# Optimization experiments

Hardware: AMD Instinct MI355X
Metric: run time of the kernel (lower is better)

Reference implementation:

```python
import jax, jax.numpy as jnp
import numpy as np
from jax import lax

STRIDES = (8, 16, 32)
NUM_CLASSES = 80
TOPK = 1000
CONF_THRESH = 0.05
NMS_THRESH = 0.6


def setup_inputs() -> dict:
    key = jax.random.key(0)
    ks = jax.random.split(key, 10)
    hw = [(256, 256), (128, 128), (64, 64)]
    inp = {}
    for lv, (h, w) in enumerate(hw):
        inp[f"cls_pred_{lv}"] = jax.random.normal(ks[3 * lv + 0], (NUM_CLASSES, h, w), jnp.float32)
        inp[f"reg_pred_{lv}"] = jax.random.normal(ks[3 * lv + 1], (4, h, w), jnp.float32)
        inp[f"ctn_pred_{lv}"] = jax.random.normal(ks[3 * lv + 2], (1, h, w), jnp.float32)
    inp["scales"] = jax.random.uniform(ks[9], (3,), jnp.float32)
    return inp


def _level_decode(cls_p, reg_p, ctn_p, scale, stride):
    # cls_p: [C,H,W] -> flatten to [M,C] matching torch permute(1,2,0).view(-1,C)
    C, H, W = cls_p.shape
    cls = jnp.transpose(cls_p, (1, 2, 0)).reshape(-1, C)          # [M,C]
    reg = jnp.transpose(reg_p, (1, 2, 0)).reshape(-1, 4)          # [M,4]
    reg = jax.nn.relu(reg * scale) * stride                       # Scale + relu + stride
    ctn = jnp.transpose(ctn_p, (1, 2, 0)).reshape(-1, 1)          # [M,1]
    joint = jnp.sqrt(jax.nn.sigmooid(cls) * jax.nn.sigmoid(ctn)) if False else \
        jnp.sqrt(jax.nn.sigmoid(cls) * jax.nn.sigmoid(ctn))      # [M,C]
    scores = jnp.max(joint, axis=-1)                              # [M]
    labels = jnp.argmax(joint, axis=-1)                           # [M]
    ay, ax = jnp.meshgrid(jnp.arange(H), jnp.arange(W), indexing='ij')
    anchors = (jnp.stack([ax, ay], -1).reshape(-1, 2).astype(cls.dtype) + 0.5) * stride  # [M,2]
    # per-level topk (M > TOPK for all levels here)
    scores, idx = lax.top_k(scores, TOPK)
    labels = labels[idx]
    reg = reg[idx]
    anchors = anchors[idx]
    boxes = jnp.concatenate([anchors - reg[:, :2], anchors + reg[:, 2:]], axis=-1)  # x1y1x2y2
    return scores, labels, boxes


def _nms(boxes, scores):
    # Faithful port of the pure-python NMS: fixed-shape keep mask, sorted order.
    N = boxes.shape[0]
    order = jnp.argsort(-scores)
    b = boxes[order]
    x1, y1, x2, y2 = b[:, 0], b[:, 1], b[:, 2], b[:, 3]
    areas = (x2 - x1) * (y2 - y1)
    xx1 = jnp.maximum(x1[:, None], x1[None, :])
    yy1 = jnp.maximum(y1[:, None], y1[None, :])
    xx2 = jnp.minimum(x2[:, None], x2[None, :])
    yy2 = jnp.minimum(y2[:, None], y2[None, :])
    w = jnp.maximum(1e-10, xx2 - xx1)
    h = jnp.maximum(1e-10, yy2 - yy1)
    inter = w * h
    iou = inter / (areas[:, None] + areas[None, :] - inter + 1e-14)  # [N,N]
    idxs = jnp.arange(N)

    def body(i, keep):
        sup = (iou[i] > NMS_THRESH) & (idxs > i) & keep[i]
        return keep & ~sup

    keep = lax.fori_loop(0, N, body, jnp.ones((N,), bool))
    return order, keep


def reference(cls_pred_0, cls_pred_1, cls_pred_2,
              reg_pred_0, reg_pred_1, reg_pred_2,
              ctn_pred_0, ctn_pred_1, ctn_pred_2, scales):
    cls_l = [cls_pred_0, cls_pred_1, cls_pred_2]
    reg_l = [reg_pred_0, reg_pred_1, reg_pred_2]
    ctn_l = [ctn_pred_0, ctn_pred_1, ctn_pred_2]
    all_s, all_l, all_b = [], [], []
    for lv in range(3):
        s, lb, bx = _level_decode(cls_l[lv], reg_l[lv], ctn_l[lv], scales[lv], float(STRIDES[lv]))
        all_s.append(s); all_l.append(lb); all_b.append(bx)
    scores = jnp.concatenate(all_s)   # [3000]
    labels = jnp.concatenate(all_l)
    boxes = jnp.concatenate(all_b)    # [3000,4]
    order, keep = _nms(boxes, scores)
    scores_s = scores[order]
    labels_s = labels[order]
    boxes_s = boxes[order]
    keep = keep & (scores_s > CONF_THRESH)
    return boxes_s, scores_s, labels_s, keep
```

## Files before the change

kernel.cpp:

```cpp
#include <hip/hip_runtime.h>
#include <cmath>
#include <stdint.h>

#define NPTS   86016
#define NCB    1024
#define K_TOP  1000
#define NOUT   3000
#define NWORDS 47
#define NTILE  47
#define ECAP   8192
#define FCAP   1024
#define SPPB   64

#define CH_OFF     0
#define CNT_OFF    (NCB * 3 * 4)
#define MEMSET_BYTES (CNT_OFF + 64)
#define KEYS_OFF   (CNT_OFF + 64)
#define LAB_OFF    (KEYS_OFF + NPTS * 8)
#define STAGE_OFF  (LAB_OFF + NPTS * 4)
#define SURV_OFF   (STAGE_OFF + 3 * 65536 * 8)
#define EDGE_OFF   (SURV_OFF + NOUT * 8 + 64)
#define FLAG_OFF   (EDGE_OFF + ECAP * 4)

__device__ __forceinline__ float sig_f32_stepwise(float x) {
    float e = (float)exp(-(double)x);
    return 1.0f / (1.0f + e);
}

__device__ __forceinline__ void locate(int g, int& lv, int& p, int& HW) {
    if (g < 65536)      { lv = 0; p = g;         HW = 65536; }
    else if (g < 81920) { lv = 1; p = g - 65536; HW = 16384; }
    else                { lv = 2; p = g - 81920; HW = 4096;  }
}

__global__ __launch_bounds__(256) void score_kernel(
        const float* __restrict__ cls0, const float* __restrict__ cls1,
        const float* __restrict__ cls2,
        const float* __restrict__ ctn0, const float* __restrict__ ctn1,
        const float* __restrict__ ctn2,
        unsigned long long* __restrict__ keys, int* __restrict__ labels,
        int* __restrict__ chist,
        int* __restrict__ cnt, unsigned* __restrict__ flags) {
    __shared__ float pm[5 * SPPB], pv[5 * SPPB];
    __shared__ int pidx[5 * SPPB];
    __shared__ int lch[NCB];
    const int tid = threadIdx.x;
    const int base = blockIdx.x * SPPB;
    for (int i = tid; i < NCB; i += 256) lch[i] = 0;
    for (int it = tid; it < 5 * SPPB; it += 256) {
        int c = it / SPPB, pt = it - c * SPPB;
        int g = base + pt, lv, p, HW;
        locate(g, lv, p, HW);
        const float* cls = (lv == 0) ? cls0 : ((lv == 1) ? cls1 : cls2);
        const float* bp = cls + (size_t)c * 16 * HW + p;
        float x[16];
#pragma unroll
        for (int cc = 0; cc < 16; cc++) x[cc] = bp[(size_t)cc * HW];
        float m = -INFINITY, v = -INFINITY; int idx = 0;
#pragma unroll
        for (int cc = 0; cc < 16; cc++)
            if (x[cc] > m) { v = m; m = x[cc]; idx = c * 16 + cc; }
        pm[it] = m; pv[it] = v; pidx[it] = idx;
    }
    __syncthreads();
    if (tid < SPPB) {
        int g = base + tid, lv, p, HW;
        locate(g, lv, p, HW);
        const float* ctn = (lv == 0) ? ctn0 : ((lv == 1) ? ctn1 : ctn2);
        float m = -INFINITY, v = -INFINITY; int idx = 0;
#pragma unroll
        for (int k = 0; k < 5; k++) {
            float bm = pm[k * SPPB + tid];
            float bv = pv[k * SPPB + tid];
            int bidx = pidx[k * SPPB + tid];
            if (bm > m) { v = fmaxf(m, bv); m = bm; idx = bidx; }
        }
        float sc = sig_f32_stepwise(ctn[p]);
        float sM = sig_f32_stepwise(m);
        float jm = __fsqrt_rn(sM * sc);
        float sV = sig_f32_stepwise(v);
        float jv = __fsqrt_rn(sV * sc);
        if (jv == jm) {
            int f = atomicAdd(&cnt[13], 1);
            if (f < FCAP) flags[f] = (unsigned)g;
        }
        unsigned int bits = __float_as_uint(jm);
        keys[g] = ((unsigned long long)bits << 32) | (0xFFFFFFFFu - (unsigned)g);
        labels[g] = idx;
        atomicAdd(&lch[(int)(bits >> 20)], 1);
    }
    __syncthreads();
    int lv0, p0, HW0; locate(base, lv0, p0, HW0);
    for (int i = tid; i < NCB; i += 256) {
        int v = lch[i];
        if (v) atomicAdd(&chist[lv0 * NCB + i], v);
    }
}

__global__ __launch_bounds__(1024) void tcs_kernel(
        const float* __restrict__ cls0, const float* __restrict__ cls1,
        const float* __restrict__ cls2,
        const float* __restrict__ ctn0, const float* __restrict__ ctn1,
        const float* __restrict__ ctn2,
        const unsigned long long* __restrict__ keys,
        const int* __restrict__ chist,
        const unsigned* __restrict__ flags, const int* __restrict__ cnt,
        int* __restrict__ labels,
        unsigned long long* __restrict__ stage,
        unsigned long long* __restrict__ surv) {
    int bid = blockIdx.x, tid = threadIdx.x;
    if (bid == 3) {
        int nf = cnt[13]; if (nf > FCAP) nf = FCAP;
        int wave = tid >> 6, lane = tid & 63;
        for (int f = wave; f < nf; f += 16) {
            int g = (int)flags[f], lv, p, HW;
            locate(g, lv, p, HW);
            const float* cls = (lv == 0) ? cls0 : ((lv == 1) ? cls1 : cls2);
            const float* ctn = (lv == 0) ? ctn0 : ((lv == 1) ? ctn1 : ctn2);
            float sc = sig_f32_stepwise(ctn[p]);
            float bestv = -1.0f; int besti = 127;
            {
                float s = sig_f32_stepwise(cls[(size_t)lane * HW + p]);
                float sj = __fsqrt_rn(s * sc);
                bestv = sj; besti = lane;
            }
            if (lane < 16) {
                int c2 = lane + 64;
                float s = sig_f32_stepwise(cls[(size_t)c2 * HW + p]);
                float sj = __fsqrt_rn(s * sc);
                if (sj > bestv) { bestv = sj; besti = c2; }
            }
            for (int off = 32; off; off >>= 1) {
                float ov = __shfl_xor(bestv, off, 64);
                int   oi = __shfl_xor(besti, off, 64);
                if (ov > bestv || (ov == bestv && oi < besti)) { bestv = ov; besti = oi; }
            }
            if (lane == 0) labels[g] = besti;
        }
        return;
    }
    const int lv = bid;
    const int base = (lv == 0) ? 0 : ((lv == 1) ? 65536 : 81920);
    const int HW = (lv == 0) ? 65536 : ((lv == 1) ? 16384 : 4096);
    unsigned long long* stg = stage + (size_t)lv * 65536;
    const int lane = tid & 63;
    const int wv = tid >> 6;
    const unsigned long long lmlt = (1ULL << lane) - 1;

    __shared__ int fine[257];
    __shared__ int wtot[16], wsuf[16];
    __shared__ int s_chunk, s_above, sBf;
    __shared__ int sSure, sStage, sCand;
    __shared__ unsigned long long sel[1024];
    __shared__ unsigned long long cbuf[1024];

    if (tid == 0) { sSure = 0; sStage = 0; sCand = 0; }
    if (tid < 257) fine[tid] = 0;

    {
        int s = chist[lv * NCB + tid];
#pragma unroll
        for (int off = 1; off <= 32; off <<= 1) {
            int t = __shfl_down(s, off, 64);
            if (lane + off < 64) s += t;
        }
        if (lane == 0) wtot[wv] = s;
        __syncthreads();
        if (tid < 16) {
            int t = wtot[tid];
#pragma unroll
            for (int off = 1; off <= 8; off <<= 1) {
                int q = __shfl_down(t, off, 64);
                if (tid + off < 16) t += q;
            }
            wsuf[tid] = t;
        }
        __syncthreads();
        int offW = (wv < 15) ? wsuf[wv + 1] : 0;
        int part_i = s + offW;
        int s1 = __shfl_down(s, 1, 64);
        int part_n = (lane < 63) ? (s1 + offW) : offW;
        if (part_i >= K_TOP && part_n < K_TOP) { s_chunk = tid; s_above = part_n; }
    }
    __syncthreads();
    const int chunk = s_chunk, above = s_above;

    {
        const int nSlab = HW >> 10;
        for (int s0 = 0; s0 < nSlab; s0 += 8) {
            unsigned long long k8[8];
#pragma unroll
            for (int u = 0; u < 8; u++)
                k8[u] = (s0 + u < nSlab) ? keys[base + ((s0 + u) << 10) + tid] : 0ULL;
#pragma unroll
            for (int u = 0; u < 8; u++) if (s0 + u < nSlab) {
                unsigned long long key = k8[u];
                int cb = (int)(key >> 52);
                bool pS = cb > chunk, pT = cb == chunk;
                unsigned long long mS = __ballot(pS);
                if (mS) {
                    int ldr = __ffsll((long long)mS) - 1;
                    int bk;
                    if (lane == ldr) bk = atomicAdd(&sSure, __popcll(mS));
                    bk = __shfl(bk, ldr, 64);
                    if (pS) sel[bk + __popcll(mS & lmlt)] = key;
                }
                unsigned long long mT = __ballot(pT);
                if (mT) {
                    int ldr = __ffsll((long long)mT) - 1;
                    int bk;
                    if (lane == ldr) bk = atomicAdd(&sStage, __popcll(mT));
                    bk = __shfl(bk, ldr, 64);
                    if (pT) {
                        stg[bk + __popcll(mT & lmlt)] = key;
                        atomicAdd(&fine[(int)(key >> 44) & 255], 1);
                    }
                }
            }
        }
    }
    __syncthreads();

    {
        int fs = (tid < 256) ? fine[tid] : 0;
#pragma unroll
        for (int off = 1; off <= 32; off <<= 1) {
            int t = __shfl_down(fs, off, 64);
            if (lane + off < 64) fs += t;
        }
        if (tid < 256 && lane == 0) wtot[wv] = fs;
        __syncthreads();
        if (tid < 4) {
            int t = wtot[tid];
#pragma unroll
            for (int off = 1; off <= 2; off <<= 1) {
                int q = __shfl_down(t, off, 64);
                if (tid + off < 4) t += q;
            }
            wsuf[tid] = t;
        }
        __syncthreads();
        if (tid < 256) {
            int offW = (wv < 3) ? wsuf[wv + 1] : 0;
            int ge = above + fs + offW;
            int fs1 = __shfl_down(fs, 1, 64);
            int genxt = above + ((lane < 63) ? (fs1 + offW) : offW);
            if (ge >= K_TOP && genxt < K_TOP) sBf = tid;
        }
    }
    __syncthreads();
    const int Bf = sBf;
    const int nst = sStage;

    for (int i0 = 0; i0 < nst; i0 += 4096) {
        unsigned long long k4[4];
#pragma unroll
        for (int u = 0; u < 4; u++) {
            int i = i0 + (u << 10) + tid;
            k4[u] = (i < nst) ? stg[i] : 0ULL;
        }
#pragma unroll
        for (int u = 0; u < 4; u++) {
            int i = i0 + (u << 10) + tid;
            bool valid = i < nst;
            unsigned long long key = k4[u];
            int fb = (int)(key >> 44) & 255;
            bool pS = valid && (fb > Bf);
            bool pC = valid && (fb == Bf);
            unsigned long long mS = __ballot(pS);
            if (mS) {
                int ldr = __ffsll((long long)mS) - 1;
                int bk;
                if (lane == ldr) bk = atomicAdd(&sSure, __popcll(mS));
                bk = __shfl(bk, ldr, 64);
                if (pS) sel[bk + __popcll(mS & lmlt)] = key;
            }
            unsigned long long mC = __ballot(pC);
            if (mC) {
                int ldr = __ffsll((long long)mC) - 1;
                int bk;
                if (lane == ldr) bk = atomicAdd(&sCand, __popcll(mC));
                bk = __shfl(bk, ldr, 64);
                if (pC) {
                    int pos = bk + __popcll(mC & lmlt);
                    if (pos < 1024) cbuf[pos] = key;
                }
            }
        }
    }
    __syncthreads();

    const int nS = sSure;
    int nC = sCand; if (nC > 1024) nC = 1024;
    unsigned long long myS = (tid < nS) ? sel[tid] : 0ULL;
    unsigned long long myC = (tid < nC) ? cbuf[tid] : 0ULL;
    int rS = 0, rC = 0;
#pragma unroll 4
    for (int i = 0; i < nS; i++) rS += (sel[i] > myS);
#pragma unroll 4
    for (int i = 0; i < nC; i++) rC += (cbuf[i] > myC);
    __syncthreads();
    if (tid < nS) sel[rS] = myS;
    if (tid < nC) cbuf[rC] = myC;
    __syncthreads();
    if (tid < K_TOP) surv[lv * K_TOP + tid] = (tid < nS) ? sel[tid] : cbuf[tid - nS];
}

__global__ __launch_bounds__(1024) void merge_emit_kernel(
        const unsigned long long* __restrict__ surv,
        const int* __restrict__ labels,
        const float* __restrict__ reg0, const float* __restrict__ reg1,
        const float* __restrict__ reg2,
        const float* __restrict__ scales,
        float* __restrict__ out) {
    __shared__ unsigned long long L[3][1024];
    __shared__ unsigned long long s[NOUT];
    int tid = threadIdx.x;
#pragma unroll
    for (int lv = 0; lv < 3; lv++)
        L[lv][tid] = (tid < K_TOP) ? surv[lv * K_TOP + tid] : 0ULL;
    __syncthreads();
    for (int e = tid; e < NOUT; e += 1024) {
        int a = e / K_TOP, i = e - a * K_TOP;
        unsigned long long key = L[a][i];
        int rank = i;
#pragma unroll
        for (int b = 0; b < 3; b++) {
            if (b == a) continue;
            int lo = 0, hi = K_TOP;
            while (lo < hi) {
                int mid = (lo + hi) >> 1;
                if (L[b][mid] > key) lo = mid + 1; else hi = mid;
            }
            rank += lo;
        }
        s[rank] = key;
    }
    __syncthreads();
    for (int r = tid; r < NOUT; r += 1024) {
        unsigned long long key = s[r];
        unsigned int bits = (unsigned)(key >> 32);
        float score = __uint_as_float(bits);
        unsigned int g = 0xFFFFFFFFu - (unsigned)(key & 0xFFFFFFFFULL);
        int lv, p;
        if (g < 65536u)      { lv = 0; p = (int)g; }
        else if (g < 81920u) { lv = 1; p = (int)g - 65536; }
        else                 { lv = 2; p = (int)g - 81920; }
        const float* rp = (lv == 0) ? reg0 : ((lv == 1) ? reg1 : reg2);
        int HW = (lv == 0) ? 65536 : ((lv == 1) ? 16384 : 4096);
        int W = 256 >> lv;
        float strideF = (float)(8 << lv);
        float scale = scales[lv];
        int x = p & (W - 1);
        int y = p >> (8 - lv);
        float r0 = fmaxf(0.0f, rp[0 * HW + p] * scale) * strideF;
        float r1 = fmaxf(0.0f, rp[1 * HW + p] * scale) * strideF;
        float r2 = fmaxf(0.0f, rp[2 * HW + p] * scale) * strideF;
        float r3 = fmaxf(0.0f, rp[3 * HW + p] * scale) * strideF;
        float ax = ((float)x + 0.5f) * strideF;
        float ay = ((float)y + 0.5f) * strideF;
        out[r * 4 + 0] = ax - r0;
        out[r * 4 + 1] = ay - r1;
        out[r * 4 + 2] = ax + r2;
        out[r * 4 + 3] = ay + r3;
        out[12000 + r] = score;
        out[15000 + r] = (float)labels[g];
    }
}

__global__ __launch_bounds__(256) void edge_kernel(const float* __restrict__ out,
                                                   unsigned* __restrict__ edges_g,
                                                   int* __restrict__ cnt) {
    __shared__ float x1[128], y1[128], x2[128], y2[128];
    int t = blockIdx.x, tid = threadIdx.x;
    int ta = 0, rem = t;
    while (rem >= NTILE - ta) { rem -= NTILE - ta; ta++; }
    int tb = ta + rem;
    if (tid < 64) {
        int gi = ta * 64 + tid;
        if (gi < NOUT) {
            float4 b = ((const float4*)out)[gi];
            x1[tid] = b.x; y1[tid] = b.y; x2[tid] = b.z; y2[tid] = b.w;
        }
    } else if (tid < 128) {
        int gj = tb * 64 + (tid - 64);
        if (gj < NOUT) {
            float4 b = ((const float4*)out)[gj];
            x1[tid] = b.x; y1[tid] = b.y; x2[tid] = b.z; y2[tid] = b.w;
        }
    }
    __syncthreads();
#pragma unroll
    for (int q = 0; q < 16; q++) {
        int idx = q * 256 + tid;
        int ii = idx >> 6, jj = idx & 63;
        int i = ta * 64 + ii, j = tb * 64 + jj;
        if (i < j && j < NOUT) {
            float ai = (x2[ii] - x1[ii]) * (y2[ii] - y1[ii]);
            float aj = (x2[64 + jj] - x1[64 + jj]) * (y2[64 + jj] - y1[64 + jj]);
            float xx1 = fmaxf(x1[ii], x1[64 + jj]), yy1 = fmaxf(y1[ii], y1[64 + jj]);
            float xx2 = fminf(x2[ii], x2[64 + jj]), yy2 = fminf(y2[ii], y2[64 + jj]);
            float ww = fmaxf(1e-10f, xx2 - xx1);
            float hh = fmaxf(1e-10f, yy2 - yy1);
            float inter = ww * hh;
            float iou = inter / (((ai + aj) - inter) + 1e-14f);
            if ((double)iou > 0.6) {
                int e = atomicAdd(&cnt[12], 1);
                if (e < ECAP) edges_g[e] = ((unsigned)i << 12) | (unsigned)j;
            }
        }
    }
}

__global__ __launch_bounds__(1024) void nms_sparse_kernel(
        const unsigned* __restrict__ edges_g,
        const int* __restrict__ cnt,
        const float* __restrict__ scores_s,
        float* __restrict__ keep_out) {
    __shared__ unsigned ed[ECAP];
    __shared__ unsigned long long supLds[NWORDS];
    int tid = threadIdx.x;
    int E = cnt[12]; if (E > ECAP) E = ECAP;
    int m = 1; while (m < E) m <<= 1;
    for (int t = tid; t < m; t += 1024) ed[t] = (t < E) ? edges_g[t] : 0xFFFFFFFFu;
    __syncthreads();
    for (int k = 2; k <= m; k <<= 1)
        for (int j = k >> 1; j > 0; j >>= 1) {
            for (int t = tid; t < m; t += 1024) {
                int l = t ^ j;
                if (l > t) {
                    unsigned a = ed[t], b = ed[l];
                    if (((t & k) == 0) ? (a > b) : (a < b)) { ed[t] = b; ed[l] = a; }
                }
            }
            __syncthreads();
        }
    if (tid < 64) {
        int lane = tid;
        unsigned long long supW = 0ULL;
        int ep = 0;
        for (int c = 0; c < NWORDS; c++) {
            unsigned long long cw = __shfl(supW, c, 64);
            int hi = (c + 1) * 64;
            while (ep < E) {
                unsigned k = ed[ep];
                int i = (int)(k >> 12);
                if (i >= hi) break;
                int j = (int)(k & 4095);
                if (!((cw >> (i & 63)) & 1ULL)) {
                    if ((j >> 6) == c) cw |= 1ULL << (j & 63);
                    else if (lane == (j >> 6)) supW |= 1ULL << (j & 63);
                }
                ep++;
            }
            if (lane == c) supW = cw;
        }
        if (lane < NWORDS) supLds[lane] = supW;
    }
    __syncthreads();
    for (int j = tid; j < NOUT; j += 1024) {
        bool s = (supLds[j >> 6] >> (j & 63)) & 1ULL;
        float scv = scores_s[j];
        keep_out[j] = (!s && ((double)scv > 0.05)) ? 1.0f : 0.0f;
    }
}

extern "C" void kernel_launch(void* const* d_in, const int* in_sizes, int n_in,
                              void* d_out, int out_size, void* d_ws, size_t ws_size,
                              hipStream_t stream) {
    const float* cls0 = (const float*)d_in[0];
    const float* reg0 = (const float*)d_in[1];
    const float* ctn0 = (const float*)d_in[2];
    const float* cls1 = (const float*)d_in[3];
    const float* reg1 = (const float*)d_in[4];
    const float* ctn1 = (const float*)d_in[5];
    const float* cls2 = (const float*)d_in[6];
    const float* reg2 = (const float*)d_in[7];
    const float* ctn2 = (const float*)d_in[8];
    const float* scales = (const float*)d_in[9];

    char* ws = (char*)d_ws;
    int* chist = (int*)(ws + CH_OFF);
    int* cnt  = (int*)(ws + CNT_OFF);
    unsigned long long* keys = (unsigned long long*)(ws + KEYS_OFF);
    int* labels = (int*)(ws + LAB_OFF);
    unsigned long long* stage = (unsigned long long*)(ws + STAGE_OFF);
    unsigned long long* surv = (unsigned long long*)(ws + SURV_OFF);
    unsigned* edges = (unsigned*)(ws + EDGE_OFF);
    unsigned* flags = (unsigned*)(ws + FLAG_OFF);
    float* out = (float*)d_out;

    hipMemsetAsync(ws, 0, MEMSET_BYTES, stream);

    score_kernel<<<NPTS / SPPB, 256, 0, stream>>>(cls0, cls1, cls2, ctn0, ctn1, ctn2,
                                                  keys, labels, chist, cnt, flags);
    tcs_kernel<<<4, 1024, 0, stream>>>(cls0, cls1, cls2, ctn0, ctn1, ctn2,
                                       keys, chist, flags, cnt, labels,
                                       stage, surv);
    merge_emit_kernel<<<1, 1024, 0, stream>>>(surv, labels, reg0, reg1, reg2, scales, out);
    edge_kernel<<<NTILE * (NTILE + 1) / 2, 256, 0, stream>>>(out, edges, cnt);
    nms_sparse_kernel<<<1, 1024, 0, stream>>>(edges, cnt, out + 12000, out + 18000);
}
```

Measured before the change: 191.8 us.

## Split top-k selection into a grid-wide scan kernel and per-level select kernel

The single-block-per-level threshold scan over all keys moves into a new 84-block scan_kernel. Each block classifies one 1024-key slab against the coarse histogram chunk and writes sure and staged keys and a fine histogram to global memory through global atomics. A separate select_kernel then reads these per-level buffers to do the fine-bucket pass and the rank sort. The rank-count loops are also rewritten with four independent accumulators. The aim is to remove the serial walk over 64K level-0 keys in one block, at the cost of an extra kernel launch, global atomics and more workspace traffic.

```diff
diff --git a/kernel.cpp b/kernel.cpp
--- a/kernel.cpp
+++ b/kernel.cpp
@@ -13,11 +13,13 @@
 #define SPPB   64
 
 #define CH_OFF     0
-#define CNT_OFF    (NCB * 3 * 4)
+#define FINE_OFF   (NCB * 3 * 4)
+#define CNT_OFF    (FINE_OFF + 3 * 256 * 4)
 #define MEMSET_BYTES (CNT_OFF + 64)
 #define KEYS_OFF   (CNT_OFF + 64)
 #define LAB_OFF    (KEYS_OFF + NPTS * 8)
-#define STAGE_OFF  (LAB_OFF + NPTS * 4)
+#define SURE_OFF   (LAB_OFF + NPTS * 4)
+#define STAGE_OFF  (SURE_OFF + 3 * 1024 * 8)
 #define SURV_OFF   (STAGE_OFF + 3 * 65536 * 8)
 #define EDGE_OFF   (SURV_OFF + NOUT * 8 + 64)
 #define FLAG_OFF   (EDGE_OFF + ECAP * 4)
@@ -97,16 +99,86 @@
     }
 }
 
-__global__ __launch_bounds__(1024) void tcs_kernel(
+__global__ __launch_bounds__(1024) void scan_kernel(
+        const unsigned long long* __restrict__ keys,
+        const int* __restrict__ chist,
+        int* __restrict__ cnt, int* __restrict__ fineg,
+        unsigned long long* __restrict__ sure,
+        unsigned long long* __restrict__ stage) {
+    const int bid = blockIdx.x, tid = threadIdx.x;
+    const int lane = tid & 63, wv = tid >> 6;
+    const unsigned long long lmlt = (1ULL << lane) - 1;
+    int lv, off;
+    if (bid < 64)      { lv = 0; off = bid << 10; }
+    else if (bid < 80) { lv = 1; off = (bid - 64) << 10; }
+    else               { lv = 2; off = (bid - 80) << 10; }
+    const int base = (lv == 0) ? 0 : ((lv == 1) ? 65536 : 81920);
+
+    __shared__ int wtot[16], wsuf[16];
+    __shared__ int s_chunk;
+
+    unsigned long long key = keys[base + off + tid];
+
+    {
+        int s = chist[lv * NCB + tid];
+#pragma unroll
+        for (int o = 1; o <= 32; o <<= 1) {
+            int t = __shfl_down(s, o, 64);
+            if (lane + o < 64) s += t;
+        }
+        if (lane == 0) wtot[wv] = s;
+        __syncthreads();
+        if (tid < 16) {
+            int t = wtot[tid];
+#pragma unroll
+            for (int o = 1; o <= 8; o <<= 1) {
+                int q = __shfl_down(t, o, 64);
+                if (tid + o < 16) t += q;
+            }
+            wsuf[tid] = t;
+        }
+        __syncthreads();
+        int offW = (wv < 15) ? wsuf[wv + 1] : 0;
+        int part_i = s + offW;
+        int s1 = __shfl_down(s, 1, 64);
+        int part_n = (lane < 63) ? (s1 + offW) : offW;
+        if (part_i >= K_TOP && part_n < K_TOP) s_chunk = tid;
+    }
+    __syncthreads();
+    const int chunk = s_chunk;
+
+    int cb = (int)(key >> 52);
+    bool pS = cb > chunk, pT = cb == chunk;
+    unsigned long long mS = __ballot(pS);
+    if (mS) {
+        int ldr = __ffsll((long long)mS) - 1;
+        int bk;
+        if (lane == ldr) bk = atomicAdd(&cnt[0 + lv], __popcll(mS));
+        bk = __shfl(bk, ldr, 64);
+        if (pS) sure[lv * 1024 + bk + __popcll(mS & lmlt)] = key;
+    }
+    unsigned long long mT = __ballot(pT);
+    if (mT) {
+        int ldr = __ffsll((long long)mT) - 1;
+        int bk;
+        if (lane == ldr) bk = atomicAdd(&cnt[3 + lv], __popcll(mT));
+        bk = __shfl(bk, ldr, 64);
+        if (pT) {
+            stage[(size_t)lv * 65536 + bk + __popcll(mT & lmlt)] = key;
+            atomicAdd(&fineg[lv * 256 + ((int)(key >> 44) & 255)], 1);
+        }
+    }
+}
+
+__global__ __launch_bounds__(1024) void select_kernel(
         const float* __restrict__ cls0, const float* __restrict__ cls1,
         const float* __restrict__ cls2,
         const float* __restrict__ ctn0, const float* __restrict__ ctn1,
         const float* __restrict__ ctn2,
-        const unsigned long long* __restrict__ keys,
-        const int* __restrict__ chist,
-        const unsigned* __restrict__ flags, const int* __restrict__ cnt,
-        int* __restrict__ labels,
-        unsigned long long* __restrict__ stage,
+        const int* __restrict__ cnt, const int* __restrict__ fineg,
+        const unsigned long long* __restrict__ sure,
+        const unsigned long long* __restrict__ stage,
+        const unsigned* __restrict__ flags, int* __restrict__ labels,
         unsigned long long* __restrict__ surv) {
     int bid = blockIdx.x, tid = threadIdx.x;
     if (bid == 3) {
@@ -140,102 +212,33 @@
         return;
     }
     const int lv = bid;
-    const int base = (lv == 0) ? 0 : ((lv == 1) ? 65536 : 81920);
-    const int HW = (lv == 0) ? 65536 : ((lv == 1) ? 16384 : 4096);
-    unsigned long long* stg = stage + (size_t)lv * 65536;
-    const int lane = tid & 63;
-    const int wv = tid >> 6;
+    const int lane = tid & 63, wv = tid >> 6;
     const unsigned long long lmlt = (1ULL << lane) - 1;
-
-    __shared__ int fine[257];
     __shared__ int wtot[16], wsuf[16];
-    __shared__ int s_chunk, s_above, sBf;
-    __shared__ int sSure, sStage, sCand;
+    __shared__ int sBf, sSure, sCand;
     __shared__ unsigned long long sel[1024];
     __shared__ unsigned long long cbuf[1024];
 
-    if (tid == 0) { sSure = 0; sStage = 0; sCand = 0; }
-    if (tid < 257) fine[tid] = 0;
+    const int above = cnt[0 + lv];
+    const int nst = cnt[3 + lv];
+    if (tid == 0) { sSure = above; sCand = 0; }
+    if (tid < above) sel[tid] = sure[lv * 1024 + tid];
 
     {
-        int s = chist[lv * NCB + tid];
-#pragma unroll
-        for (int off = 1; off <= 32; off <<= 1) {
-            int t = __shfl_down(s, off, 64);
-            if (lane + off < 64) s += t;
-        }
-        if (lane == 0) wtot[wv] = s;
-        __syncthreads();
-        if (tid < 16) {
-            int t = wtot[tid];
-#pragma unroll
-            for (int off = 1; off <= 8; off <<= 1) {
-                int q = __shfl_down(t, off, 64);
-                if (tid + off < 16) t += q;
-            }
-            wsuf[tid] = t;
-        }
-        __syncthreads();
-        int offW = (wv < 15) ? wsuf[wv + 1] : 0;
-        int part_i = s + offW;
-        int s1 = __shfl_down(s, 1, 64);
-        int part_n = (lane < 63) ? (s1 + offW) : offW;
-        if (part_i >= K_TOP && part_n < K_TOP) { s_chunk = tid; s_above = part_n; }
-    }
-    __syncthreads();
-    const int chunk = s_chunk, above = s_above;
-
-    {
-        const int nSlab = HW >> 10;
-        for (int s0 = 0; s0 < nSlab; s0 += 8) {
-            unsigned long long k8[8];
-#pragma unroll
-            for (int u = 0; u < 8; u++)
-                k8[u] = (s0 + u < nSlab) ? keys[base + ((s0 + u) << 10) + tid] : 0ULL;
-#pragma unroll
-            for (int u = 0; u < 8; u++) if (s0 + u < nSlab) {
-                unsigned long long key = k8[u];
-                int cb = (int)(key >> 52);
-                bool pS = cb > chunk, pT = cb == chunk;
-                unsigned long long mS = __ballot(pS);
-                if (mS) {
-                    int ldr = __ffsll((long long)mS) - 1;
-                    int bk;
-                    if (lane == ldr) bk = atomicAdd(&sSure, __popcll(mS));
-                    bk = __shfl(bk, ldr, 64);
-                    if (pS) sel[bk + __popcll(mS & lmlt)] = key;
-                }
-                unsigned long long mT = __ballot(pT);
-                if (mT) {
-                    int ldr = __ffsll((long long)mT) - 1;
-                    int bk;
-                    if (lane == ldr) bk = atomicAdd(&sStage, __popcll(mT));
-                    bk = __shfl(bk, ldr, 64);
-                    if (pT) {
-                        stg[bk + __popcll(mT & lmlt)] = key;
-                        atomicAdd(&fine[(int)(key >> 44) & 255], 1);
-                    }
-                }
-            }
-        }
-    }
-    __syncthreads();
-
-    {
-        int fs = (tid < 256) ? fine[tid] : 0;
-#pragma unroll
-        for (int off = 1; off <= 32; off <<= 1) {
-            int t = __shfl_down(fs, off, 64);
-            if (lane + off < 64) fs += t;
+        int fs = (tid < 256) ? fineg[lv * 256 + tid] : 0;
+#pragma unroll
+        for (int o = 1; o <= 32; o <<= 1) {
+            int t = __shfl_down(fs, o, 64);
+            if (lane + o < 64) fs += t;
         }
         if (tid < 256 && lane == 0) wtot[wv] = fs;
         __syncthreads();
         if (tid < 4) {
             int t = wtot[tid];
 #pragma unroll
-            for (int off = 1; off <= 2; off <<= 1) {
-                int q = __shfl_down(t, off, 64);
-                if (tid + off < 4) t += q;
+            for (int o = 1; o <= 2; o <<= 1) {
+                int q = __shfl_down(t, o, 64);
+                if (tid + o < 4) t += q;
             }
             wsuf[tid] = t;
         }
@@ -250,41 +253,32 @@
     }
     __syncthreads();
     const int Bf = sBf;
-    const int nst = sStage;
-
-    for (int i0 = 0; i0 < nst; i0 += 4096) {
-        unsigned long long k4[4];
-#pragma unroll
-        for (int u = 0; u < 4; u++) {
-            int i = i0 + (u << 10) + tid;
-            k4[u] = (i < nst) ? stg[i] : 0ULL;
-        }
-#pragma unroll
-        for (int u = 0; u < 4; u++) {
-            int i = i0 + (u << 10) + tid;
-            bool valid = i < nst;
-            unsigned long long key = k4[u];
-            int fb = (int)(key >> 44) & 255;
-            bool pS = valid && (fb > Bf);
-            bool pC = valid && (fb == Bf);
-            unsigned long long mS = __ballot(pS);
-            if (mS) {
-                int ldr = __ffsll((long long)mS) - 1;
-                int bk;
-                if (lane == ldr) bk = atomicAdd(&sSure, __popcll(mS));
-                bk = __shfl(bk, ldr, 64);
-                if (pS) sel[bk + __popcll(mS & lmlt)] = key;
-            }
-            unsigned long long mC = __ballot(pC);
-            if (mC) {
-                int ldr = __ffsll((long long)mC) - 1;
-                int bk;
-                if (lane == ldr) bk = atomicAdd(&sCand, __popcll(mC));
-                bk = __shfl(bk, ldr, 64);
-                if (pC) {
-                    int pos = bk + __popcll(mC & lmlt);
-                    if (pos < 1024) cbuf[pos] = key;
-                }
+
+    for (int i0 = tid; ; i0 += 1024) {
+        bool any = (i0 - tid) < nst;
+        if (!any) break;
+        bool valid = i0 < nst;
+        unsigned long long key = valid ? stage[(size_t)lv * 65536 + i0] : 0ULL;
+        int fb = (int)(key >> 44) & 255;
+        bool pS = valid && (fb > Bf);
+        bool pC = valid && (fb == Bf);
+        unsigned long long mS = __ballot(pS);
+        if (mS) {
+            int ldr = __ffsll((long long)mS) - 1;
+            int bk;
+            if (lane == ldr) bk = atomicAdd(&sSure, __popcll(mS));
+            bk = __shfl(bk, ldr, 64);
+            if (pS) sel[bk + __popcll(mS & lmlt)] = key;
+        }
+        unsigned long long mC = __ballot(pC);
+        if (mC) {
+            int ldr = __ffsll((long long)mC) - 1;
+            int bk;
+            if (lane == ldr) bk = atomicAdd(&sCand, __popcll(mC));
+            bk = __shfl(bk, ldr, 64);
+            if (pC) {
+                int pos = bk + __popcll(mC & lmlt);
+                if (pos < 1024) cbuf[pos] = key;
             }
         }
     }
@@ -294,11 +288,22 @@
     int nC = sCand; if (nC > 1024) nC = 1024;
     unsigned long long myS = (tid < nS) ? sel[tid] : 0ULL;
     unsigned long long myC = (tid < nC) ? cbuf[tid] : 0ULL;
-    int rS = 0, rC = 0;
-#pragma unroll 4
-    for (int i = 0; i < nS; i++) rS += (sel[i] > myS);
-#pragma unroll 4
-    for (int i = 0; i < nC; i++) rC += (cbuf[i] > myC);
+    int a0 = 0, a1 = 0, a2 = 0, a3 = 0;
+    int i = 0;
+    for (; i + 4 <= nS; i += 4) {
+        a0 += (sel[i] > myS); a1 += (sel[i + 1] > myS);
+        a2 += (sel[i + 2] > myS); a3 += (sel[i + 3] > myS);
+    }
+    for (; i < nS; i++) a0 += (sel[i] > myS);
+    int rS = a0 + a1 + a2 + a3;
+    int b0 = 0, b1 = 0, b2 = 0, b3 = 0;
+    i = 0;
+    for (; i + 4 <= nC; i += 4) {
+        b0 += (cbuf[i] > myC); b1 += (cbuf[i + 1] > myC);
+        b2 += (cbuf[i + 2] > myC); b3 += (cbuf[i + 3] > myC);
+    }
+    for (; i < nC; i++) b0 += (cbuf[i] > myC);
+    int rC = b0 + b1 + b2 + b3;
     __syncthreads();
     if (tid < nS) sel[rS] = myS;
     if (tid < nC) cbuf[rC] = myC;
@@ -481,9 +486,11 @@
 
     char* ws = (char*)d_ws;
     int* chist = (int*)(ws + CH_OFF);
+    int* fineg = (int*)(ws + FINE_OFF);
     int* cnt  = (int*)(ws + CNT_OFF);
     unsigned long long* keys = (unsigned long long*)(ws + KEYS_OFF);
     int* labels = (int*)(ws + LAB_OFF);
+    unsigned long long* sure = (unsigned long long*)(ws + SURE_OFF);
     unsigned long long* stage = (unsigned long long*)(ws + STAGE_OFF);
     unsigned long long* surv = (unsigned long long*)(ws + SURV_OFF);
     unsigned* edges = (unsigned*)(ws + EDGE_OFF);
@@ -494,9 +501,9 @@
 
     score_kernel<<<NPTS / SPPB, 256, 0, stream>>>(cls0, cls1, cls2, ctn0, ctn1, ctn2,
                                                   keys, labels, chist, cnt, flags);
-    tcs_kernel<<<4, 1024, 0, stream>>>(cls0, cls1, cls2, ctn0, ctn1, ctn2,
-                                       keys, chist, flags, cnt, labels,
-                                       stage, surv);
+    scan_kernel<<<84, 1024, 0, stream>>>(keys, chist, cnt, fineg, sure, stage);
+    select_kernel<<<4, 1024, 0, stream>>>(cls0, cls1, cls2, ctn0, ctn1, ctn2,
+                                          cnt, fineg, sure, stage, flags, labels, surv);
     merge_emit_kernel<<<1, 1024, 0, stream>>>(surv, labels, reg0, reg1, reg2, scales, out);
     edge_kernel<<<NTILE * (NTILE + 1) / 2, 256, 0, stream>>>(out, edges, cnt);
     nms_sparse_kernel<<<1, 1024, 0, stream>>>(edges, cnt, out + 12000, out + 18000);
```

New measurement: 182.8 us. 1.05x faster.
